# Kernel optimization log

Hardware: AMD Instinct MI355X
Metric: run time of the kernel (lower is better)

## Reference

```python
import jax, jax.numpy as jnp
import numpy as np

N = 400000   # nodes; must equal E because the original code computes `out + x` with out per-edge
E = 400000   # edges
HID = 128
HEADS = 4
NEG_SLOPE = 0.01  # torch F.leaky_relu default


def setup_inputs() -> dict:
    key = jax.random.key(0)
    k1, k2, k3, k4 = jax.random.split(key, 4)
    x = jax.random.normal(k1, (N, HID), dtype=jnp.float32)
    edge_index = jax.random.randint(k2, (2, E), 0, N, dtype=jnp.int64)
    # xavier-uniform-ish scale for the attention parameter [1, heads, 2*hidden]
    lim_a = float(np.sqrt(6.0 / (1 + HEADS * 2 * HID)))
    attention = jax.random.uniform(k3, (1, HEADS, 2 * HID), jnp.float32, -lim_a, lim_a)
    lim_w = float(np.sqrt(1.0 / (HID * HEADS)))
    W = jax.random.uniform(k4, (HID, HID * HEADS), jnp.float32, -lim_w, lim_w)
    b = jnp.zeros((HID,), jnp.float32)
    return {"x": x, "edge_index": edge_index, "attention": attention, "W": W, "b": b}


def _scatter_softmax(s, seg, num_segments):
    # softmax over edges grouped by destination node index `seg` (axis 0)
    m = jax.lax.stop_gradient(jax.ops.segment_max(s, seg, num_segments=num_segments))
    ex = jnp.exp(s - m[seg])
    denom = jax.ops.segment_sum(ex, seg, num_segments=num_segments)
    return ex / denom[seg]


def reference(x, edge_index, attention, W, b):
    row, col = edge_index[0], edge_index[1]
    # [E, 2*HID] per-edge concatenated features
    ef = jnp.concatenate([x[row], x[col]], axis=-1)
    # per-head scores: (ef[:,None,:] * attention).sum(-1) -> [E, HEADS]
    scores = jnp.einsum('ef,hf->eh', ef, attention[0])
    scores = jax.nn.leaky_relu(scores, NEG_SLOPE)
    scores = jax.nn.softmax(scores, axis=1)      # softmax across heads (as in source)
    # dropout(p=0.1) -> identity in eval mode
    alpha = _scatter_softmax(scores, row, N)     # [E, HEADS] per-destination softmax
    # per-head weighted source features, concatenated over heads -> [E, HEADS*HID]
    feats = (alpha[:, :, None] * x[col][:, None, :]).reshape(E, HEADS * HID)
    out = feats @ W.T + b                        # Linear(hidden*heads -> hidden)
    return out + x
```

## Files before the change

### kernel.cpp

```cpp
#include <hip/hip_runtime.h>

#define NN 400000
#define NE 400000

typedef __attribute__((ext_vector_type(4))) float f32x4;
typedef __attribute__((ext_vector_type(8))) short s16x8;
typedef unsigned short ushort_t;

__device__ __forceinline__ ushort_t f2bf(float f) {
    union { float f; unsigned int u; } c;
    c.f = f;
    unsigned int u = c.u;
    u = u + 0x7fffu + ((u >> 16) & 1u);
    return (ushort_t)(u >> 16);
}
__device__ __forceinline__ float bf2f(ushort_t v) {
    union { unsigned int u; float f; } c;
    c.u = ((unsigned int)v) << 16;
    return c.f;
}

__global__ void k_detect(const int* __restrict__ ei_raw, int* __restrict__ flag) {
    if (threadIdx.x == 0 && blockIdx.x == 0) {
        int is64 = 1;
        for (int i = 0; i < 64; i++)
            if (ei_raw[2 * i + 1] != 0) { is64 = 0; break; }
        flag[0] = is64;
    }
}

__global__ void k_cvt_idx(const int* __restrict__ ei_raw, const int* __restrict__ flag,
                          int* __restrict__ ei32) {
    const int i = blockIdx.x * 256 + threadIdx.x;
    const int f = flag[0];
    ei32[i] = f ? ei_raw[2 * i] : ei_raw[i];
}

__global__ void k_wcvt(const float* __restrict__ W, ushort_t* __restrict__ wbf) {
    const int i = blockIdx.x * 256 + threadIdx.x;
    wbf[i] = f2bf(W[i]);
}

__global__ void k_uv_cvt(const float* __restrict__ x, const float* __restrict__ att,
                         ushort_t* __restrict__ xbf, float* __restrict__ uv) {
    const int lane = threadIdx.x & 63;
    const int wid = threadIdx.x >> 6;
    const int g = lane & 15;
    const int ns = lane >> 4;

    float areg[8][8];
#pragma unroll
    for (int h = 0; h < 4; h++) {
        const f32x4 fa = *(const f32x4*)(att + h * 256 + g * 8);
        const f32x4 fb = *(const f32x4*)(att + h * 256 + g * 8 + 4);
        const f32x4 ba = *(const f32x4*)(att + h * 256 + 128 + g * 8);
        const f32x4 bb = *(const f32x4*)(att + h * 256 + 128 + g * 8 + 4);
#pragma unroll
        for (int m = 0; m < 4; m++) {
            areg[h][m] = fa[m];     areg[h][4 + m] = fb[m];
            areg[4 + h][m] = ba[m]; areg[4 + h][4 + m] = bb[m];
        }
    }

    for (int tile = blockIdx.x; tile < NN / 32; tile += gridDim.x) {
        const int nb = tile * 32 + wid * 8 + ns;
#pragma unroll
        for (int t = 0; t < 2; t++) {
            const int n = nb + t * 4;
            const f32x4 xa = *(const f32x4*)(x + (size_t)n * 128 + g * 8);
            const f32x4 xb = *(const f32x4*)(x + (size_t)n * 128 + g * 8 + 4);
            s16x8 pk;
#pragma unroll
            for (int m = 0; m < 4; m++) { pk[m] = (short)f2bf(xa[m]); pk[4 + m] = (short)f2bf(xb[m]); }
            *(s16x8*)(xbf + (size_t)n * 128 + g * 8) = pk;
            float r[8];
#pragma unroll
            for (int v = 0; v < 8; v++) {
                float s = 0.f;
#pragma unroll
                for (int m = 0; m < 4; m++) s += xa[m] * areg[v][m];
#pragma unroll
                for (int m = 0; m < 4; m++) s += xb[m] * areg[v][4 + m];
                r[v] = s;
            }
#pragma unroll
            for (int mask = 1; mask <= 4; mask <<= 1)
#pragma unroll
                for (int v = 0; v < 8; v++) r[v] += __shfl_xor(r[v], mask, 64);
            const int gv = g & 7;
            float s = r[0];
#pragma unroll
            for (int v = 1; v < 8; v++) s = (gv == v) ? r[v] : s;
            s += __shfl_xor(s, 8, 64);
            if (g < 8) uv[(size_t)n * 8 + g] = s;
        }
    }
}

__global__ void k_edge(const int* __restrict__ ei, const float* __restrict__ uv,
                       float* __restrict__ p, float* __restrict__ denom) {
    const int e = blockIdx.x * 256 + threadIdx.x;
    if (e >= NE) return;
    const int row = ei[e];
    const int col = ei[NE + e];
    const f32x4 u = *(const f32x4*)(uv + (size_t)row * 8);
    const f32x4 v = *(const f32x4*)(uv + (size_t)col * 8 + 4);
    float s[4];
    float mx = -1e30f;
#pragma unroll
    for (int h = 0; h < 4; h++) {
        float t = u[h] + v[h];
        t = t > 0.f ? t : 0.01f * t;
        s[h] = t;
        mx = fmaxf(mx, t);
    }
    float ex[4], sum = 0.f;
#pragma unroll
    for (int h = 0; h < 4; h++) { ex[h] = __expf(s[h] - mx); sum += ex[h]; }
    const float inv = 1.f / sum;
    f32x4 pv;
#pragma unroll
    for (int h = 0; h < 4; h++) pv[h] = __expf(ex[h] * inv);
    *(f32x4*)(p + (size_t)e * 4) = pv;
#pragma unroll
    for (int h = 0; h < 4; h++) atomicAdd(denom + (size_t)row * 4 + h, pv[h]);
}

__global__ __launch_bounds__(256, 2) void k_gemm(
    const ushort_t* __restrict__ xbf, const int* __restrict__ ei,
    const float* __restrict__ p, const float* __restrict__ denom,
    const ushort_t* __restrict__ wbf, const float* __restrict__ bias,
    float* __restrict__ out)
{
    __shared__ __align__(16) ushort_t Asm[128 * 128];
    __shared__ __align__(16) float alp_s[4][128];

    const int tid = threadIdx.x;
    const int lane = tid & 63;
    const int w = tid >> 6;
    const int e0 = blockIdx.x * 128;

    {
#pragma unroll
        for (int i = 0; i < 8; i++) {
            const int rr = w * 32 + i * 4 + (lane >> 4);
            const int col = ei[NE + e0 + rr];
            const int c = (lane & 15) ^ (rr & 15);
            const ushort_t* src = xbf + (size_t)col * 128 + c * 8;
            __builtin_amdgcn_global_load_lds(
                (const __attribute__((address_space(1))) unsigned int*)src,
                (__attribute__((address_space(3))) unsigned int*)((char*)Asm + w * 8192 + i * 1024),
                16, 0, 0);
        }
    }
    if (tid < 128) {
        const int e = e0 + tid;
        const int row = ei[e];
        const f32x4 pv = *(const f32x4*)(p + (size_t)e * 4);
        const f32x4 dv = *(const f32x4*)(denom + (size_t)row * 4);
#pragma unroll
        for (int h = 0; h < 4; h++) alp_s[h][tid] = pv[h] / dv[h];
    }
    s16x8 bfr[4][4][2];
#pragma unroll
    for (int cb = 0; cb < 2; cb++) {
        const ushort_t* bbase = wbf + (size_t)(w * 32 + cb * 16 + (lane & 15)) * 512 + (lane >> 4) * 8;
#pragma unroll
        for (int h = 0; h < 4; h++)
#pragma unroll
            for (int ks = 0; ks < 4; ks++)
                bfr[h][ks][cb] = *(const s16x8*)(bbase + h * 128 + ks * 32);
    }
    float bias_r[2];
#pragma unroll
    for (int cb = 0; cb < 2; cb++) bias_r[cb] = bias[w * 32 + cb * 16 + (lane & 15)];

    __syncthreads();

    const f32x4 zero = {0.f, 0.f, 0.f, 0.f};

#pragma unroll 1
    for (int t = 0; t < 4; t++) {
        s16x8 af[2][4];
#pragma unroll
        for (int eb = 0; eb < 2; eb++) {
            const int rr = t * 32 + eb * 16 + (lane & 15);
#pragma unroll
            for (int ks = 0; ks < 4; ks++) {
                const int byte = rr * 256 + ((ks * 64 + (lane >> 4) * 16) ^ ((rr & 15) << 4));
                af[eb][ks] = *(const s16x8*)((const char*)Asm + byte);
            }
        }
        f32x4 fin[2][2];
#pragma unroll
        for (int eb = 0; eb < 2; eb++)
#pragma unroll
            for (int cb = 0; cb < 2; cb++) fin[eb][cb] = zero;

#pragma unroll
        for (int h = 0; h < 4; h++) {
            f32x4 av[2];
#pragma unroll
            for (int eb = 0; eb < 2; eb++)
                av[eb] = *(const f32x4*)&alp_s[h][t * 32 + eb * 16 + (lane >> 4) * 4];
#pragma unroll
            for (int eb = 0; eb < 2; eb++)
#pragma unroll
                for (int cb = 0; cb < 2; cb++) {
                    f32x4 a = __builtin_amdgcn_mfma_f32_16x16x32_bf16(af[eb][0], bfr[h][0][cb], zero, 0, 0, 0);
#pragma unroll
                    for (int ks = 1; ks < 4; ks++)
                        a = __builtin_amdgcn_mfma_f32_16x16x32_bf16(af[eb][ks], bfr[h][ks][cb], a, 0, 0, 0);
                    fin[eb][cb] += av[eb] * a;
                }
        }
#pragma unroll
        for (int eb = 0; eb < 2; eb++)
#pragma unroll
            for (int cb = 0; cb < 2; cb++) {
                const int i = w * 32 + cb * 16 + (lane & 15);
#pragma unroll
                for (int r = 0; r < 4; r++) {
                    const int e = e0 + t * 32 + eb * 16 + (lane >> 4) * 4 + r;
                    const size_t off = (size_t)e * 128 + i;
                    out[off] = fin[eb][cb][r] + bias_r[cb] + bf2f(xbf[off]);
                }
            }
    }
}

extern "C" void kernel_launch(void* const* d_in, const int* in_sizes, int n_in,
                              void* d_out, int out_size, void* d_ws, size_t ws_size,
                              hipStream_t stream) {
    const float* x      = (const float*)d_in[0];
    const int*   ei_raw = (const int*)d_in[1];
    const float* att    = (const float*)d_in[2];
    const float* W      = (const float*)d_in[3];
    const float* b      = (const float*)d_in[4];
    float* out = (float*)d_out;

    char* ws = (char*)d_ws;
    float*    uv      = (float*)(ws);
    float*    p       = (float*)(ws + 12800000);
    float*    denom   = (float*)(ws + 19200000);
    ushort_t* wbf     = (ushort_t*)(ws + 32000000);
    int*      flag    = (int*)(ws + 32200000);
    int*      ei32    = (int*)(ws + 32200064);
    ushort_t* xbf     = (ushort_t*)(ws + 35400192);

    hipMemsetAsync(denom, 0, (size_t)NN * 4 * sizeof(float), stream);
    k_detect<<<1, 64, 0, stream>>>(ei_raw, flag);
    k_cvt_idx<<<2 * NE / 256, 256, 0, stream>>>(ei_raw, flag, ei32);
    k_wcvt<<<256, 256, 0, stream>>>(W, wbf);
    k_uv_cvt<<<2048, 256, 0, stream>>>(x, att, xbf, uv);
    k_edge<<<(NE + 255) / 256, 256, 0, stream>>>(ei32, uv, p, denom);
    k_gemm<<<NE / 128, 256, 0, stream>>>(xbf, ei32, p, denom, wbf, b, out);
}
```

Before: 285.1 us.

## Make GEMM persistent with W staged once in LDS per block

The GEMM kernel becomes persistent: 256 blocks of 512 threads loop over 64-edge tiles. The full bf16 W (128x512) is loaded once per block into swizzled LDS instead of being reloaded into registers by every one of the 3125 blocks. The goal is to cut repeated W global traffic and register pressure. In exchange, B fragments are now read from LDS on every tile, a block uses about 145KB of LDS which limits occupancy, and there are two barriers per tile with no overlap between the gather and the compute.

```diff
diff --git a/kernel.cpp b/kernel.cpp
--- a/kernel.cpp
+++ b/kernel.cpp
@@ -126,104 +126,119 @@
     for (int h = 0; h < 4; h++) atomicAdd(denom + (size_t)row * 4 + h, pv[h]);
 }
 
-__global__ __launch_bounds__(256, 2) void k_gemm(
+__global__ __launch_bounds__(512, 2) void k_gemm(
     const ushort_t* __restrict__ xbf, const int* __restrict__ ei,
     const float* __restrict__ p, const float* __restrict__ denom,
     const ushort_t* __restrict__ wbf, const float* __restrict__ bias,
     float* __restrict__ out)
 {
-    __shared__ __align__(16) ushort_t Asm[128 * 128];
-    __shared__ __align__(16) float alp_s[4][128];
+    __shared__ __align__(16) ushort_t Bsm[128 * 512];
+    __shared__ __align__(16) ushort_t Asm[64 * 128];
+    __shared__ __align__(16) float alp_s[4][64];
 
     const int tid = threadIdx.x;
     const int lane = tid & 63;
     const int w = tid >> 6;
-    const int e0 = blockIdx.x * 128;
+    const int eg = w & 1;
+    const int cg = w >> 1;
 
     {
-#pragma unroll
-        for (int i = 0; i < 8; i++) {
-            const int rr = w * 32 + i * 4 + (lane >> 4);
-            const int col = ei[NE + e0 + rr];
+        const int icol = tid >> 2, q = tid & 3;
+        const ushort_t* src = wbf + icol * 512 + q * 128;
+#pragma unroll
+        for (int m = 0; m < 16; m++) {
+            const s16x8 v = *(const s16x8*)(src + m * 8);
+            const int lb = q * 256 + m * 16;
+            const int byte = icol * 1024 + (lb ^ ((icol & 7) << 4));
+            *(s16x8*)((char*)Bsm + byte) = v;
+        }
+    }
+    float bias_r[2];
+#pragma unroll
+    for (int cbi = 0; cbi < 2; cbi++) bias_r[cbi] = bias[cg * 32 + cbi * 16 + (lane & 15)];
+
+    const f32x4 zero = {0.f, 0.f, 0.f, 0.f};
+    const int ntiles = NE / 64;
+
+#pragma unroll 1
+    for (int tile = blockIdx.x; tile < ntiles; tile += gridDim.x) {
+        __syncthreads();
+#pragma unroll
+        for (int i = 0; i < 2; i++) {
+            const int rr = w * 8 + i * 4 + (lane >> 4);
+            const int col = ei[NE + tile * 64 + rr];
             const int c = (lane & 15) ^ (rr & 15);
             const ushort_t* src = xbf + (size_t)col * 128 + c * 8;
             __builtin_amdgcn_global_load_lds(
                 (const __attribute__((address_space(1))) unsigned int*)src,
-                (__attribute__((address_space(3))) unsigned int*)((char*)Asm + w * 8192 + i * 1024),
+                (__attribute__((address_space(3))) unsigned int*)((char*)Asm + w * 2048 + i * 1024),
                 16, 0, 0);
         }
-    }
-    if (tid < 128) {
-        const int e = e0 + tid;
-        const int row = ei[e];
-        const f32x4 pv = *(const f32x4*)(p + (size_t)e * 4);
-        const f32x4 dv = *(const f32x4*)(denom + (size_t)row * 4);
-#pragma unroll
-        for (int h = 0; h < 4; h++) alp_s[h][tid] = pv[h] / dv[h];
-    }
-    s16x8 bfr[4][4][2];
-#pragma unroll
-    for (int cb = 0; cb < 2; cb++) {
-        const ushort_t* bbase = wbf + (size_t)(w * 32 + cb * 16 + (lane & 15)) * 512 + (lane >> 4) * 8;
-#pragma unroll
-        for (int h = 0; h < 4; h++)
-#pragma unroll
-            for (int ks = 0; ks < 4; ks++)
-                bfr[h][ks][cb] = *(const s16x8*)(bbase + h * 128 + ks * 32);
-    }
-    float bias_r[2];
-#pragma unroll
-    for (int cb = 0; cb < 2; cb++) bias_r[cb] = bias[w * 32 + cb * 16 + (lane & 15)];
-
-    __syncthreads();
-
-    const f32x4 zero = {0.f, 0.f, 0.f, 0.f};
-
-#pragma unroll 1
-    for (int t = 0; t < 4; t++) {
+        if (tid < 64) {
+            const int e = tile * 64 + tid;
+            const int row = ei[e];
+            const f32x4 pv = *(const f32x4*)(p + (size_t)e * 4);
+            const f32x4 dv = *(const f32x4*)(denom + (size_t)row * 4);
+#pragma unroll
+            for (int h = 0; h < 4; h++) alp_s[h][tid] = pv[h] / dv[h];
+        }
+        __syncthreads();
+
         s16x8 af[2][4];
 #pragma unroll
         for (int eb = 0; eb < 2; eb++) {
-            const int rr = t * 32 + eb * 16 + (lane & 15);
+            const int rr = eg * 32 + eb * 16 + (lane & 15);
 #pragma unroll
             for (int ks = 0; ks < 4; ks++) {
                 const int byte = rr * 256 + ((ks * 64 + (lane >> 4) * 16) ^ ((rr & 15) << 4));
                 af[eb][ks] = *(const s16x8*)((const char*)Asm + byte);
             }
         }
+
         f32x4 fin[2][2];
 #pragma unroll
         for (int eb = 0; eb < 2; eb++)
 #pragma unroll
-            for (int cb = 0; cb < 2; cb++) fin[eb][cb] = zero;
+            for (int cbi = 0; cbi < 2; cbi++) fin[eb][cbi] = zero;
 
 #pragma unroll
         for (int h = 0; h < 4; h++) {
+            s16x8 bfr[2][4];
+#pragma unroll
+            for (int cbi = 0; cbi < 2; cbi++) {
+                const int icol = cg * 32 + cbi * 16 + (lane & 15);
+#pragma unroll
+                for (int ks = 0; ks < 4; ks++) {
+                    const int byte = icol * 1024 +
+                        ((h * 256 + ks * 64 + (lane >> 4) * 16) ^ ((icol & 7) << 4));
+                    bfr[cbi][ks] = *(const s16x8*)((const char*)Bsm + byte);
+                }
+            }
             f32x4 av[2];
 #pragma unroll
             for (int eb = 0; eb < 2; eb++)
-                av[eb] = *(const f32x4*)&alp_s[h][t * 32 + eb * 16 + (lane >> 4) * 4];
+                av[eb] = *(const f32x4*)&alp_s[h][eg * 32 + eb * 16 + (lane >> 4) * 4];
 #pragma unroll
             for (int eb = 0; eb < 2; eb++)
 #pragma unroll
-                for (int cb = 0; cb < 2; cb++) {
-                    f32x4 a = __builtin_amdgcn_mfma_f32_16x16x32_bf16(af[eb][0], bfr[h][0][cb], zero, 0, 0, 0);
+                for (int cbi = 0; cbi < 2; cbi++) {
+                    f32x4 a = __builtin_amdgcn_mfma_f32_16x16x32_bf16(af[eb][0], bfr[cbi][0], zero, 0, 0, 0);
 #pragma unroll
                     for (int ks = 1; ks < 4; ks++)
-                        a = __builtin_amdgcn_mfma_f32_16x16x32_bf16(af[eb][ks], bfr[h][ks][cb], a, 0, 0, 0);
-                    fin[eb][cb] += av[eb] * a;
+                        a = __builtin_amdgcn_mfma_f32_16x16x32_bf16(af[eb][ks], bfr[cbi][ks], a, 0, 0, 0);
+                    fin[eb][cbi] += av[eb] * a;
                 }
         }
 #pragma unroll
         for (int eb = 0; eb < 2; eb++)
 #pragma unroll
-            for (int cb = 0; cb < 2; cb++) {
-                const int i = w * 32 + cb * 16 + (lane & 15);
+            for (int cbi = 0; cbi < 2; cbi++) {
+                const int icol = cg * 32 + cbi * 16 + (lane & 15);
 #pragma unroll
                 for (int r = 0; r < 4; r++) {
-                    const int e = e0 + t * 32 + eb * 16 + (lane >> 4) * 4 + r;
-                    const size_t off = (size_t)e * 128 + i;
-                    out[off] = fin[eb][cb][r] + bias_r[cb] + bf2f(xbf[off]);
+                    const int e = tile * 64 + eg * 32 + eb * 16 + (lane >> 4) * 4 + r;
+                    const size_t off = (size_t)e * 128 + icol;
+                    out[off] = fin[eb][cbi][r] + bias_r[cbi] + bf2f(xbf[off]);
                 }
             }
     }
@@ -254,5 +269,5 @@
     k_wcvt<<<256, 256, 0, stream>>>(W, wbf);
     k_uv_cvt<<<2048, 256, 0, stream>>>(x, att, xbf, uv);
     k_edge<<<(NE + 255) / 256, 256, 0, stream>>>(ei32, uv, p, denom);
-    k_gemm<<<NE / 128, 256, 0, stream>>>(xbf, ei32, p, denom, wbf, b, out);
-}
+    k_gemm<<<256, 512, 0, stream>>>(xbf, ei32, p, denom, wbf, b, out);
+}
```

Result: no change. 279.7 us (-1.9%).
